# Performance work log

Hardware: AMD Instinct MI355X
Metric: run time of the kernel (lower is better)

## Reference

```python
import jax, jax.numpy as jnp
import numpy as np

WINDOW_SIZE = 11
SIGMA = 1.5
C1 = 0.01 ** 2
C2 = 0.03 ** 2


def _gaussian_window(window_size, num_channels, dtype=jnp.float32):
    x = np.arange(window_size)
    k = np.exp(-((x - window_size // 2) ** 2) / (2.0 * SIGMA ** 2))
    k = k / k.sum()
    k2d = np.outer(k, k).astype(np.float32)
    # (C, 1, K, K) depthwise kernel, same Gaussian per channel
    w = np.broadcast_to(k2d, (num_channels, 1, window_size, window_size))
    return jnp.asarray(np.ascontiguousarray(w), dtype=dtype)


def _depthwise_conv(x, window):
    # x: (N,C,H,W), window: (C,1,K,K); groups=C, SAME-ish padding = K//2
    pad = window.shape[-1] // 2
    return jax.lax.conv_general_dilated(
        x, window,
        window_strides=(1, 1),
        padding=[(pad, pad), (pad, pad)],
        dimension_numbers=("NCHW", "OIHW", "NCHW"),
        feature_group_count=x.shape[1],
    )


def setup_inputs() -> dict:
    key = jax.random.key(0)
    k1, k2 = jax.random.split(key)
    shape = (16, 3, 512, 512)
    img1 = jax.random.uniform(k1, shape, dtype=jnp.float32)
    img2 = jax.random.uniform(k2, shape, dtype=jnp.float32)
    window = _gaussian_window(WINDOW_SIZE, shape[1])
    return {"img1": img1, "img2": img2, "window": window}


def reference(img1, img2, window):
    mu1 = _depthwise_conv(img1, window)
    mu2 = _depthwise_conv(img2, window)
    mu1_sq = mu1 * mu1
    mu2_sq = mu2 * mu2
    mu1_mu2 = mu1 * mu2
    sigma1_sq = _depthwise_conv(img1 * img1, window) - mu1_sq
    sigma2_sq = _depthwise_conv(img2 * img2, window) - mu2_sq
    sigma12 = _depthwise_conv(img1 * img2, window) - mu1_mu2
    ssim_map = ((2.0 * mu1_mu2 + C1) * (2.0 * sigma12 + C2)) / (
        (mu1_sq + mu2_sq + C1) * (sigma1_sq + sigma2_sq + C2)
    )
    return jnp.mean(ssim_map)  # size_average=True
```

## Files before the change

### kernel.cpp

```cpp
#include <hip/hip_runtime.h>


#define KSZ   11
#define PAD   5
#define TILE  32
#define HALO  (TILE + KSZ - 1)
#define NTHREADS 256

__global__ __launch_bounds__(NTHREADS) void ssim_zero_acc(double* acc) {
    if (threadIdx.x == 0 && blockIdx.x == 0) acc[0] = 0.0;
}

__global__ __launch_bounds__(NTHREADS)
void ssim_main(const float* __restrict__ img1,
               const float* __restrict__ img2,
               const float* __restrict__ window,
               double* __restrict__ acc,
               int H, int W)
{
    __shared__ float k1d[KSZ];
    __shared__ float sx1[HALO][HALO];
    __shared__ float sx2[HALO][HALO];
    __shared__ float h0[HALO][TILE];
    __shared__ float h1[HALO][TILE];
    __shared__ float h2[HALO][TILE];
    __shared__ float h3[HALO][TILE];
    __shared__ float h4[HALO][TILE];
    __shared__ float red[NTHREADS / 64];

    const int tid = threadIdx.x;
    const int bx  = blockIdx.x * TILE;
    const int by  = blockIdx.y * TILE;
    const size_t planeOff = (size_t)blockIdx.z * H * W;
    const float* p1 = img1 + planeOff;
    const float* p2 = img2 + planeOff;

    if (tid < KSZ) {
        float s = 0.f;
        #pragma unroll
        for (int j = 0; j < KSZ; ++j) s += window[tid * KSZ + j];
        k1d[tid] = s;
    }

    for (int idx = tid; idx < HALO * HALO; idx += NTHREADS) {
        const int r = idx / HALO, c = idx % HALO;
        const int gr = by + r - PAD, gc = bx + c - PAD;
        float v1 = 0.f, v2 = 0.f;
        if (gr >= 0 && gr < H && gc >= 0 && gc < W) {
            const size_t g = (size_t)gr * W + gc;
            v1 = p1[g];
            v2 = p2[g];
        }
        sx1[r][c] = v1;
        sx2[r][c] = v2;
    }
    __syncthreads();

    for (int idx = tid; idx < HALO * TILE; idx += NTHREADS) {
        const int r = idx / TILE, c = idx % TILE;
        float a0 = 0.f, a1 = 0.f, a2 = 0.f, a3 = 0.f, a4 = 0.f;
        #pragma unroll
        for (int k = 0; k < KSZ; ++k) {
            const float w  = k1d[k];
            const float x1 = sx1[r][c + k];
            const float x2 = sx2[r][c + k];
            a0 += w * x1;
            a1 += w * x2;
            a2 += w * (x1 * x1);
            a3 += w * (x2 * x2);
            a4 += w * (x1 * x2);
        }
        h0[r][c] = a0; h1[r][c] = a1; h2[r][c] = a2; h3[r][c] = a3; h4[r][c] = a4;
    }
    __syncthreads();

    const float C1 = 1e-4f;
    const float C2 = 9e-4f;
    float lsum = 0.f;
    for (int idx = tid; idx < TILE * TILE; idx += NTHREADS) {
        const int r = idx / TILE, c = idx % TILE;
        float mu1 = 0.f, mu2 = 0.f, e11 = 0.f, e22 = 0.f, e12 = 0.f;
        #pragma unroll
        for (int k = 0; k < KSZ; ++k) {
            const float w = k1d[k];
            mu1 += w * h0[r + k][c];
            mu2 += w * h1[r + k][c];
            e11 += w * h2[r + k][c];
            e22 += w * h3[r + k][c];
            e12 += w * h4[r + k][c];
        }
        const float mu1_sq = mu1 * mu1;
        const float mu2_sq = mu2 * mu2;
        const float mu1mu2 = mu1 * mu2;
        const float s11 = e11 - mu1_sq;
        const float s22 = e22 - mu2_sq;
        const float s12 = e12 - mu1mu2;
        const float num = (2.f * mu1mu2 + C1) * (2.f * s12 + C2);
        const float den = (mu1_sq + mu2_sq + C1) * (s11 + s22 + C2);
        lsum += num / den;
    }

    #pragma unroll
    for (int off = 32; off > 0; off >>= 1)
        lsum += __shfl_down(lsum, off, 64);
    const int wave = tid >> 6;
    const int lane = tid & 63;
    if (lane == 0) red[wave] = lsum;
    __syncthreads();
    if (tid == 0) {
        float bsum = 0.f;
        #pragma unroll
        for (int w = 0; w < NTHREADS / 64; ++w) bsum += red[w];
        atomicAdd(acc, (double)bsum);
    }
}

__global__ __launch_bounds__(64) void ssim_finalize(const double* acc, float* out, double invN) {
    if (threadIdx.x == 0 && blockIdx.x == 0) out[0] = (float)(acc[0] * invN);
}

extern "C" void kernel_launch(void* const* d_in, const int* in_sizes, int n_in,
                              void* d_out, int out_size, void* d_ws, size_t ws_size,
                              hipStream_t stream) {
    const float* img1   = (const float*)d_in[0];
    const float* img2   = (const float*)d_in[1];
    const float* window = (const float*)d_in[2];
    float* out = (float*)d_out;
    double* acc = (double*)d_ws;

    const int N = 16, C = 3, H = 512, W = 512;
    const long long total = (long long)N * C * H * W;

    ssim_zero_acc<<<1, NTHREADS, 0, stream>>>(acc);

    dim3 grid(W / TILE, H / TILE, N * C);
    ssim_main<<<grid, NTHREADS, 0, stream>>>(img1, img2, window, acc, H, W);

    ssim_finalize<<<1, 64, 0, stream>>>(acc, out, 1.0 / (double)total);
}
```

Before: 263.0 us.

## Register-block separable SSIM passes and fuse finalize via last-block counter

Restructures the horizontal pass so each thread computes four adjacent outputs from float4 shared-memory loads, precomputing the squared and product terms once per input element. The vertical pass now has each thread produce four rows with sliding register accumulators, and the five intermediates are packed as a float4 plus a scalar. It uses a hardware reciprocal instead of division, replaces the zero and finalize kernels with a memset plus a last-block-done counter, and hardcodes the image dimensions. This is meant to cut LDS traffic, redundant multiplies and launch overhead, at the cost of higher register pressure and slightly less accurate division.

```diff
diff --git a/kernel.cpp b/kernel.cpp
--- a/kernel.cpp
+++ b/kernel.cpp
@@ -5,33 +5,40 @@
 #define PAD   5
 #define TILE  32
 #define HALO  (TILE + KSZ - 1)
-#define NTHREADS 256
+#define SXW   44
+#define NT    256
+#define NBX   (512 / TILE)
+#define NBY   (512 / TILE)
+#define NPLANES 48
+#define NBLOCKS (NBX * NBY * NPLANES)
 
-__global__ __launch_bounds__(NTHREADS) void ssim_zero_acc(double* acc) {
-    if (threadIdx.x == 0 && blockIdx.x == 0) acc[0] = 0.0;
+static __device__ __forceinline__ float fast_rcp(float x) {
+#if __has_builtin(__builtin_amdgcn_rcpf)
+    return __builtin_amdgcn_rcpf(x);
+#else
+    return 1.0f / x;
+#endif
 }
 
-__global__ __launch_bounds__(NTHREADS)
-void ssim_main(const float* __restrict__ img1,
-               const float* __restrict__ img2,
-               const float* __restrict__ window,
-               double* __restrict__ acc,
-               int H, int W)
+__global__ __launch_bounds__(NT)
+void ssim_fused(const float* __restrict__ img1,
+                const float* __restrict__ img2,
+                const float* __restrict__ window,
+                double* __restrict__ acc,
+                unsigned int* __restrict__ counter,
+                float* __restrict__ out)
 {
     __shared__ float k1d[KSZ];
-    __shared__ float sx1[HALO][HALO];
-    __shared__ float sx2[HALO][HALO];
-    __shared__ float h0[HALO][TILE];
-    __shared__ float h1[HALO][TILE];
-    __shared__ float h2[HALO][TILE];
-    __shared__ float h3[HALO][TILE];
-    __shared__ float h4[HALO][TILE];
-    __shared__ float red[NTHREADS / 64];
+    __shared__ __align__(16) float sx1[HALO * SXW];
+    __shared__ __align__(16) float sx2[HALO * SXW];
+    __shared__ float4 hA[HALO * TILE];
+    __shared__ float  hB[HALO * TILE];
+    __shared__ float red[NT / 64];
 
     const int tid = threadIdx.x;
-    const int bx  = blockIdx.x * TILE;
-    const int by  = blockIdx.y * TILE;
-    const size_t planeOff = (size_t)blockIdx.z * H * W;
+    const int bx = blockIdx.x * TILE;
+    const int by = blockIdx.y * TILE;
+    const size_t planeOff = (size_t)blockIdx.z * 512 * 512;
     const float* p1 = img1 + planeOff;
     const float* p2 = img2 + planeOff;
 
@@ -42,62 +49,117 @@
         k1d[tid] = s;
     }
 
-    for (int idx = tid; idx < HALO * HALO; idx += NTHREADS) {
-        const int r = idx / HALO, c = idx % HALO;
-        const int gr = by + r - PAD, gc = bx + c - PAD;
+    for (int idx = tid; idx < HALO * HALO; idx += NT) {
+        const int r = idx / HALO;
+        const int c = idx - r * HALO;
+        const int gr = by + r - PAD;
+        const int gc = bx + c - PAD;
         float v1 = 0.f, v2 = 0.f;
-        if (gr >= 0 && gr < H && gc >= 0 && gc < W) {
-            const size_t g = (size_t)gr * W + gc;
+        if (((unsigned)gr < 512u) && ((unsigned)gc < 512u)) {
+            const size_t g = (size_t)gr * 512 + gc;
             v1 = p1[g];
             v2 = p2[g];
         }
-        sx1[r][c] = v1;
-        sx2[r][c] = v2;
+        sx1[r * SXW + c] = v1;
+        sx2[r * SXW + c] = v2;
     }
     __syncthreads();
 
-    for (int idx = tid; idx < HALO * TILE; idx += NTHREADS) {
-        const int r = idx / TILE, c = idx % TILE;
-        float a0 = 0.f, a1 = 0.f, a2 = 0.f, a3 = 0.f, a4 = 0.f;
+    float wk[KSZ];
+    #pragma unroll
+    for (int k = 0; k < KSZ; ++k) wk[k] = k1d[k];
+
+    {
+        const int hcg = tid & 7;
+        const int hr0 = tid >> 3;
         #pragma unroll
-        for (int k = 0; k < KSZ; ++k) {
-            const float w  = k1d[k];
-            const float x1 = sx1[r][c + k];
-            const float x2 = sx2[r][c + k];
-            a0 += w * x1;
-            a1 += w * x2;
-            a2 += w * (x1 * x1);
-            a3 += w * (x2 * x2);
-            a4 += w * (x1 * x2);
+        for (int rr = 0; rr < 2; ++rr) {
+            const int r = hr0 + rr * 32;
+            if (r < HALO) {
+                const float4* r1 = (const float4*)(sx1 + r * SXW);
+                const float4* r2 = (const float4*)(sx2 + r * SXW);
+                const float4 A0 = r1[hcg], A1 = r1[hcg + 1], A2 = r1[hcg + 2], A3 = r1[hcg + 3];
+                const float4 B0 = r2[hcg], B1 = r2[hcg + 1], B2 = r2[hcg + 2], B3 = r2[hcg + 3];
+                const float x1v[16] = {A0.x,A0.y,A0.z,A0.w, A1.x,A1.y,A1.z,A1.w,
+                                       A2.x,A2.y,A2.z,A2.w, A3.x,A3.y,A3.z,A3.w};
+                const float x2v[16] = {B0.x,B0.y,B0.z,B0.w, B1.x,B1.y,B1.z,B1.w,
+                                       B2.x,B2.y,B2.z,B2.w, B3.x,B3.y,B3.z,B3.w};
+                float q1[14], q2[14], q12[14];
+                #pragma unroll
+                for (int i = 0; i < 14; ++i) {
+                    q1[i]  = x1v[i] * x1v[i];
+                    q2[i]  = x2v[i] * x2v[i];
+                    q12[i] = x1v[i] * x2v[i];
+                }
+                float h0[4] = {0,0,0,0}, h1[4] = {0,0,0,0}, h2[4] = {0,0,0,0},
+                      h3[4] = {0,0,0,0}, h4[4] = {0,0,0,0};
+                #pragma unroll
+                for (int k = 0; k < KSZ; ++k) {
+                    const float w = wk[k];
+                    #pragma unroll
+                    for (int c = 0; c < 4; ++c) {
+                        h0[c] += w * x1v[c + k];
+                        h1[c] += w * x2v[c + k];
+                        h2[c] += w * q1[c + k];
+                        h3[c] += w * q2[c + k];
+                        h4[c] += w * q12[c + k];
+                    }
+                }
+                const int base = r * TILE + hcg * 4;
+                #pragma unroll
+                for (int c = 0; c < 4; ++c) {
+                    hA[base + c] = make_float4(h0[c], h1[c], h2[c], h3[c]);
+                    hB[base + c] = h4[c];
+                }
+            }
         }
-        h0[r][c] = a0; h1[r][c] = a1; h2[r][c] = a2; h3[r][c] = a3; h4[r][c] = a4;
     }
     __syncthreads();
 
-    const float C1 = 1e-4f;
-    const float C2 = 9e-4f;
+    const float C1f = 1e-4f;
+    const float C2f = 9e-4f;
     float lsum = 0.f;
-    for (int idx = tid; idx < TILE * TILE; idx += NTHREADS) {
-        const int r = idx / TILE, c = idx % TILE;
-        float mu1 = 0.f, mu2 = 0.f, e11 = 0.f, e22 = 0.f, e12 = 0.f;
+    {
+        const int vc  = tid & 31;
+        const int vr0 = (tid >> 5) * 4;
+        float av[4][5];
         #pragma unroll
-        for (int k = 0; k < KSZ; ++k) {
-            const float w = k1d[k];
-            mu1 += w * h0[r + k][c];
-            mu2 += w * h1[r + k][c];
-            e11 += w * h2[r + k][c];
-            e22 += w * h3[r + k][c];
-            e12 += w * h4[r + k][c];
+        for (int i = 0; i < 4; ++i)
+            #pragma unroll
+            for (int f = 0; f < 5; ++f) av[i][f] = 0.f;
+
+        #pragma unroll
+        for (int j = 0; j < TILE - TILE + 14; ++j) {
+            const int hr = vr0 + j;
+            const float4 va = hA[hr * TILE + vc];
+            const float  vb = hB[hr * TILE + vc];
+            #pragma unroll
+            for (int i = 0; i < 4; ++i) {
+                const int k = j - i;
+                if (k >= 0 && k < KSZ) {
+                    const float w = wk[k];
+                    av[i][0] += w * va.x;
+                    av[i][1] += w * va.y;
+                    av[i][2] += w * va.z;
+                    av[i][3] += w * va.w;
+                    av[i][4] += w * vb;
+                }
+            }
         }
-        const float mu1_sq = mu1 * mu1;
-        const float mu2_sq = mu2 * mu2;
-        const float mu1mu2 = mu1 * mu2;
-        const float s11 = e11 - mu1_sq;
-        const float s22 = e22 - mu2_sq;
-        const float s12 = e12 - mu1mu2;
-        const float num = (2.f * mu1mu2 + C1) * (2.f * s12 + C2);
-        const float den = (mu1_sq + mu2_sq + C1) * (s11 + s22 + C2);
-        lsum += num / den;
+        #pragma unroll
+        for (int i = 0; i < 4; ++i) {
+            const float mu1 = av[i][0], mu2 = av[i][1];
+            const float e11 = av[i][2], e22 = av[i][3], e12 = av[i][4];
+            const float mu1sq = mu1 * mu1;
+            const float mu2sq = mu2 * mu2;
+            const float mu12  = mu1 * mu2;
+            const float s11 = e11 - mu1sq;
+            const float s22 = e22 - mu2sq;
+            const float s12 = e12 - mu12;
+            const float num = (2.f * mu12 + C1f) * (2.f * s12 + C2f);
+            const float den = (mu1sq + mu2sq + C1f) * (s11 + s22 + C2f);
+            lsum += num * fast_rcp(den);
+        }
     }
 
     #pragma unroll
@@ -108,15 +170,16 @@
     if (lane == 0) red[wave] = lsum;
     __syncthreads();
     if (tid == 0) {
-        float bsum = 0.f;
-        #pragma unroll
-        for (int w = 0; w < NTHREADS / 64; ++w) bsum += red[w];
+        float bsum = red[0] + red[1] + red[2] + red[3];
         atomicAdd(acc, (double)bsum);
+        __threadfence();
+        const unsigned prev = atomicAdd(counter, 1u);
+        if (prev == (unsigned)(NBLOCKS - 1)) {
+            __threadfence();
+            const double total = atomicAdd(acc, 0.0);
+            out[0] = (float)(total * (1.0 / ((double)NBLOCKS * TILE * TILE)));
+        }
     }
-}
-
-__global__ __launch_bounds__(64) void ssim_finalize(const double* acc, float* out, double invN) {
-    if (threadIdx.x == 0 && blockIdx.x == 0) out[0] = (float)(acc[0] * invN);
 }
 
 extern "C" void kernel_launch(void* const* d_in, const int* in_sizes, int n_in,
@@ -127,14 +190,10 @@
     const float* window = (const float*)d_in[2];
     float* out = (float*)d_out;
     double* acc = (double*)d_ws;
+    unsigned int* counter = (unsigned int*)((char*)d_ws + 8);
 
-    const int N = 16, C = 3, H = 512, W = 512;
-    const long long total = (long long)N * C * H * W;
+    hipMemsetAsync(d_ws, 0, 16, stream);
 
-    ssim_zero_acc<<<1, NTHREADS, 0, stream>>>(acc);
-
-    dim3 grid(W / TILE, H / TILE, N * C);
-    ssim_main<<<grid, NTHREADS, 0, stream>>>(img1, img2, window, acc, H, W);
-
-    ssim_finalize<<<1, 64, 0, stream>>>(acc, out, 1.0 / (double)total);
+    dim3 grid(NBX, NBY, NPLANES);
+    ssim_fused<<<grid, NT, 0, stream>>>(img1, img2, window, acc, counter, out);
 }
```

New measurement: 438.7 us. +66.8%, slower.

## Stream row bands with register-rotated vertical Gaussian accumulators

Applied to the files above, without the earlier changes.

Replaces the 32x32 tile kernel with a column-strip, row-band streaming kernel. Each thread owns one output column and keeps 11 rows of horizontal-filter partials in rotating registers, so halo rows are reused along the band and the shared intermediate planes are dropped. Also interleaves img1/img2 as float2 in shared memory, uses a hardware reciprocal instead of division, and zeroes the accumulator with a memset. The cost is high register pressure and fewer blocks (960), which may hurt occupancy; the approximate reciprocal slightly changes numerics.

```diff
diff --git a/kernel.cpp b/kernel.cpp
--- a/kernel.cpp
+++ b/kernel.cpp
@@ -2,38 +2,40 @@
 
 
 #define KSZ   11
-#define PAD   5
-#define TILE  32
-#define HALO  (TILE + KSZ - 1)
-#define NTHREADS 256
+#define NT    256
+#define BAND  56
+#define NGROUP 6
+#define SEG   544
+#define NSTG  (11 * SEG)
 
-__global__ __launch_bounds__(NTHREADS) void ssim_zero_acc(double* acc) {
-    if (threadIdx.x == 0 && blockIdx.x == 0) acc[0] = 0.0;
+struct W11 { float w[KSZ]; };
+
+static __device__ __forceinline__ float fast_rcp(float x) {
+#if __has_builtin(__builtin_amdgcn_rcpf)
+    return __builtin_amdgcn_rcpf(x);
+#else
+    return 1.0f / x;
+#endif
 }
 
-__global__ __launch_bounds__(NTHREADS)
-void ssim_main(const float* __restrict__ img1,
-               const float* __restrict__ img2,
-               const float* __restrict__ window,
-               double* __restrict__ acc,
-               int H, int W)
+__global__ __launch_bounds__(NT, 4)
+void ssim_stream(const float* __restrict__ img1,
+                 const float* __restrict__ img2,
+                 const float* __restrict__ window,
+                 double* __restrict__ acc)
 {
     __shared__ float k1d[KSZ];
-    __shared__ float sx1[HALO][HALO];
-    __shared__ float sx2[HALO][HALO];
-    __shared__ float h0[HALO][TILE];
-    __shared__ float h1[HALO][TILE];
-    __shared__ float h2[HALO][TILE];
-    __shared__ float h3[HALO][TILE];
-    __shared__ float h4[HALO][TILE];
-    __shared__ float red[NTHREADS / 64];
+    __shared__ __align__(16) float buf[11 * SEG];
+    __shared__ float red[NT / 64];
 
-    const int tid = threadIdx.x;
-    const int bx  = blockIdx.x * TILE;
-    const int by  = blockIdx.y * TILE;
-    const size_t planeOff = (size_t)blockIdx.z * H * W;
-    const float* p1 = img1 + planeOff;
-    const float* p2 = img2 + planeOff;
+    const int tid   = threadIdx.x;
+    const int strip = blockIdx.x;
+    const int band  = blockIdx.y;
+    const int plane = blockIdx.z;
+    const int R0    = band * BAND;
+    const int cbase = strip * 256 - 5;
+    const float* p1 = img1 + (size_t)plane * 512 * 512;
+    const float* p2 = img2 + (size_t)plane * 512 * 512;
 
     if (tid < KSZ) {
         float s = 0.f;
@@ -41,64 +43,110 @@
         for (int j = 0; j < KSZ; ++j) s += window[tid * KSZ + j];
         k1d[tid] = s;
     }
-
-    for (int idx = tid; idx < HALO * HALO; idx += NTHREADS) {
-        const int r = idx / HALO, c = idx % HALO;
-        const int gr = by + r - PAD, gc = bx + c - PAD;
-        float v1 = 0.f, v2 = 0.f;
-        if (gr >= 0 && gr < H && gc >= 0 && gc < W) {
-            const size_t g = (size_t)gr * W + gc;
-            v1 = p1[g];
-            v2 = p2[g];
-        }
-        sx1[r][c] = v1;
-        sx2[r][c] = v2;
-    }
     __syncthreads();
 
-    for (int idx = tid; idx < HALO * TILE; idx += NTHREADS) {
-        const int r = idx / TILE, c = idx % TILE;
-        float a0 = 0.f, a1 = 0.f, a2 = 0.f, a3 = 0.f, a4 = 0.f;
-        #pragma unroll
-        for (int k = 0; k < KSZ; ++k) {
-            const float w  = k1d[k];
-            const float x1 = sx1[r][c + k];
-            const float x2 = sx2[r][c + k];
-            a0 += w * x1;
-            a1 += w * x2;
-            a2 += w * (x1 * x1);
-            a3 += w * (x2 * x2);
-            a4 += w * (x1 * x2);
+    W11 wk;
+    #pragma unroll
+    for (int k = 0; k < KSZ; ++k) wk.w[k] = k1d[k];
+
+#define DECL(S) float S##m1=0.f, S##m2=0.f, S##e1=0.f, S##e2=0.f, S##d=0.f;
+    DECL(r0) DECL(r1) DECL(r2) DECL(r3) DECL(r4) DECL(r5)
+    DECL(r6) DECL(r7) DECL(r8) DECL(r9) DECL(r10)
+#undef DECL
+
+    const float C1f = 1e-4f;
+    const float C2f = 9e-4f;
+    float lsum = 0.f;
+
+#define HT(K)                                                           \
+    {                                                                   \
+        const float2 v = rp[K];                                         \
+        const float  w = wk.w[K];                                       \
+        hm1 += w * v.x;       hm2 += w * v.y;                           \
+        he1 += w * v.x * v.x; he2 += w * v.y * v.y;                     \
+        hd  += w * v.x * v.y;                                           \
+    }
+
+#define STEP(J, S0,S1,S2,S3,S4,S5,S6,S7,S8,S9,S10)                      \
+    {                                                                   \
+        float hm1=0.f, hm2=0.f, he1=0.f, he2=0.f, hd=0.f;               \
+        {                                                               \
+            const float2* rp = ((const float2*)(buf + (J) * SEG)) + tid;\
+            HT(0) HT(1) HT(2) HT(3) HT(4) HT(5)                         \
+            HT(6) HT(7) HT(8) HT(9) HT(10)                              \
+        }                                                               \
+        S10##m1 = hm1; S10##m2 = hm2; S10##e1 = he1;                    \
+        S10##e2 = he2; S10##d  = hd;                                    \
+        const int s_ = g * 11 + (J);                                    \
+        if (s_ >= 10) {                                                 \
+            const int orow = R0 + s_ - 10;                              \
+            if (orow < 512) {                                           \
+                const float vm1 = wk.w[0]*S0##m1 + wk.w[1]*S1##m1       \
+                  + wk.w[2]*S2##m1 + wk.w[3]*S3##m1 + wk.w[4]*S4##m1    \
+                  + wk.w[5]*S5##m1 + wk.w[6]*S6##m1 + wk.w[7]*S7##m1    \
+                  + wk.w[8]*S8##m1 + wk.w[9]*S9##m1 + wk.w[10]*S10##m1; \
+                const float vm2 = wk.w[0]*S0##m2 + wk.w[1]*S1##m2       \
+                  + wk.w[2]*S2##m2 + wk.w[3]*S3##m2 + wk.w[4]*S4##m2    \
+                  + wk.w[5]*S5##m2 + wk.w[6]*S6##m2 + wk.w[7]*S7##m2    \
+                  + wk.w[8]*S8##m2 + wk.w[9]*S9##m2 + wk.w[10]*S10##m2; \
+                const float ve1 = wk.w[0]*S0##e1 + wk.w[1]*S1##e1       \
+                  + wk.w[2]*S2##e1 + wk.w[3]*S3##e1 + wk.w[4]*S4##e1    \
+                  + wk.w[5]*S5##e1 + wk.w[6]*S6##e1 + wk.w[7]*S7##e1    \
+                  + wk.w[8]*S8##e1 + wk.w[9]*S9##e1 + wk.w[10]*S10##e1; \
+                const float ve2 = wk.w[0]*S0##e2 + wk.w[1]*S1##e2       \
+                  + wk.w[2]*S2##e2 + wk.w[3]*S3##e2 + wk.w[4]*S4##e2    \
+                  + wk.w[5]*S5##e2 + wk.w[6]*S6##e2 + wk.w[7]*S7##e2    \
+                  + wk.w[8]*S8##e2 + wk.w[9]*S9##e2 + wk.w[10]*S10##e2; \
+                const float vd  = wk.w[0]*S0##d + wk.w[1]*S1##d         \
+                  + wk.w[2]*S2##d + wk.w[3]*S3##d + wk.w[4]*S4##d       \
+                  + wk.w[5]*S5##d + wk.w[6]*S6##d + wk.w[7]*S7##d       \
+                  + wk.w[8]*S8##d + wk.w[9]*S9##d + wk.w[10]*S10##d;    \
+                const float mu1sq = vm1 * vm1;                          \
+                const float mu2sq = vm2 * vm2;                          \
+                const float mu12  = vm1 * vm2;                          \
+                const float s11 = ve1 - mu1sq;                          \
+                const float s22 = ve2 - mu2sq;                          \
+                const float s12 = vd  - mu12;                           \
+                const float num = (2.f*mu12 + C1f) * (2.f*s12 + C2f);   \
+                const float den = (mu1sq + mu2sq + C1f)                 \
+                                * (s11 + s22 + C2f);                    \
+                lsum += num * fast_rcp(den);                            \
+            }                                                           \
+        }                                                               \
+    }
+
+    for (int g = 0; g < NGROUP; ++g) {
+        for (int idx = tid; idx < NSTG; idx += NT) {
+            const int rj  = idx / SEG;
+            const int rem = idx - rj * SEG;
+            const int im  = rem / 272;
+            const int col = rem - im * 272;
+            const int prow = R0 - 5 + g * 11 + rj;
+            const int gcol = cbase + col;
+            float v = 0.f;
+            if (((unsigned)prow < 512u) && ((unsigned)gcol < 512u) && (col < 266)) {
+                const float* p = im ? p2 : p1;
+                v = p[prow * 512 + gcol];
+            }
+            buf[rj * SEG + col * 2 + im] = v;
         }
-        h0[r][c] = a0; h1[r][c] = a1; h2[r][c] = a2; h3[r][c] = a3; h4[r][c] = a4;
+        __syncthreads();
+
+        STEP(0,  r1,r2,r3,r4,r5,r6,r7,r8,r9,r10,r0)
+        STEP(1,  r2,r3,r4,r5,r6,r7,r8,r9,r10,r0,r1)
+        STEP(2,  r3,r4,r5,r6,r7,r8,r9,r10,r0,r1,r2)
+        STEP(3,  r4,r5,r6,r7,r8,r9,r10,r0,r1,r2,r3)
+        STEP(4,  r5,r6,r7,r8,r9,r10,r0,r1,r2,r3,r4)
+        STEP(5,  r6,r7,r8,r9,r10,r0,r1,r2,r3,r4,r5)
+        STEP(6,  r7,r8,r9,r10,r0,r1,r2,r3,r4,r5,r6)
+        STEP(7,  r8,r9,r10,r0,r1,r2,r3,r4,r5,r6,r7)
+        STEP(8,  r9,r10,r0,r1,r2,r3,r4,r5,r6,r7,r8)
+        STEP(9,  r10,r0,r1,r2,r3,r4,r5,r6,r7,r8,r9)
+        STEP(10, r0,r1,r2,r3,r4,r5,r6,r7,r8,r9,r10)
+        __syncthreads();
     }
-    __syncthreads();
-
-    const float C1 = 1e-4f;
-    const float C2 = 9e-4f;
-    float lsum = 0.f;
-    for (int idx = tid; idx < TILE * TILE; idx += NTHREADS) {
-        const int r = idx / TILE, c = idx % TILE;
-        float mu1 = 0.f, mu2 = 0.f, e11 = 0.f, e22 = 0.f, e12 = 0.f;
-        #pragma unroll
-        for (int k = 0; k < KSZ; ++k) {
-            const float w = k1d[k];
-            mu1 += w * h0[r + k][c];
-            mu2 += w * h1[r + k][c];
-            e11 += w * h2[r + k][c];
-            e22 += w * h3[r + k][c];
-            e12 += w * h4[r + k][c];
-        }
-        const float mu1_sq = mu1 * mu1;
-        const float mu2_sq = mu2 * mu2;
-        const float mu1mu2 = mu1 * mu2;
-        const float s11 = e11 - mu1_sq;
-        const float s22 = e22 - mu2_sq;
-        const float s12 = e12 - mu1mu2;
-        const float num = (2.f * mu1mu2 + C1) * (2.f * s12 + C2);
-        const float den = (mu1_sq + mu2_sq + C1) * (s11 + s22 + C2);
-        lsum += num / den;
-    }
+#undef STEP
+#undef HT
 
     #pragma unroll
     for (int off = 32; off > 0; off >>= 1)
@@ -108,15 +156,15 @@
     if (lane == 0) red[wave] = lsum;
     __syncthreads();
     if (tid == 0) {
-        float bsum = 0.f;
-        #pragma unroll
-        for (int w = 0; w < NTHREADS / 64; ++w) bsum += red[w];
+        const float bsum = red[0] + red[1] + red[2] + red[3];
         atomicAdd(acc, (double)bsum);
     }
 }
 
-__global__ __launch_bounds__(64) void ssim_finalize(const double* acc, float* out, double invN) {
-    if (threadIdx.x == 0 && blockIdx.x == 0) out[0] = (float)(acc[0] * invN);
+__global__ __launch_bounds__(64)
+void ssim_finalize(const double* __restrict__ acc, float* __restrict__ out) {
+    if (threadIdx.x == 0)
+        out[0] = (float)(acc[0] * (1.0 / 12582912.0));
 }
 
 extern "C" void kernel_launch(void* const* d_in, const int* in_sizes, int n_in,
@@ -128,13 +176,9 @@
     float* out = (float*)d_out;
     double* acc = (double*)d_ws;
 
-    const int N = 16, C = 3, H = 512, W = 512;
-    const long long total = (long long)N * C * H * W;
+    hipMemsetAsync(d_ws, 0, 8, stream);
 
-    ssim_zero_acc<<<1, NTHREADS, 0, stream>>>(acc);
-
-    dim3 grid(W / TILE, H / TILE, N * C);
-    ssim_main<<<grid, NTHREADS, 0, stream>>>(img1, img2, window, acc, H, W);
-
-    ssim_finalize<<<1, 64, 0, stream>>>(acc, out, 1.0 / (double)total);
+    dim3 grid(2, 10, 48);
+    ssim_stream<<<grid, NT, 0, stream>>>(img1, img2, window, acc);
+    ssim_finalize<<<1, 64, 0, stream>>>(acc, out);
 }
```

Result: slower. 280.7 us (+6.7%).
